# Kernel optimization log

Hardware: AMD Instinct MI355X
Metric: run time of the kernel (lower is better)

## Reference

```python
import jax, jax.numpy as jnp
import numpy as np

N_NODES = 50000
N_EDGES = 800000
IN_DIM = 128
HIDDEN_DIM = 128


def setup_inputs() -> dict:
    key = jax.random.key(0)
    k1, k2, k3, k4 = jax.random.split(key, 4)
    x = jax.random.normal(k1, (N_NODES, IN_DIM), dtype=jnp.float32)
    edge_index = jax.random.randint(k2, (2, N_EDGES), 0, N_NODES, dtype=jnp.int64)
    # Glorot-ish init for weights
    W1 = jax.random.normal(k3, (IN_DIM, HIDDEN_DIM), dtype=jnp.float32) / np.sqrt(IN_DIM)
    b1 = jnp.zeros((HIDDEN_DIM,), dtype=jnp.float32)
    W2 = jax.random.normal(k4, (HIDDEN_DIM, 2), dtype=jnp.float32) / np.sqrt(HIDDEN_DIM)
    b2 = jnp.zeros((2,), dtype=jnp.float32)
    return {"x": x, "edge_index": edge_index, "W1": W1, "b1": b1, "W2": W2, "b2": b2}


def _gcn_norm(edge_index, n_nodes):
    """Add self-loops and compute symmetric GCN normalization per edge."""
    loops = jnp.arange(n_nodes, dtype=edge_index.dtype)
    src = jnp.concatenate([edge_index[0], loops])  # [E + N]
    dst = jnp.concatenate([edge_index[1], loops])  # [E + N]
    ones = jnp.ones_like(dst, dtype=jnp.float32)
    deg = jax.ops.segment_sum(ones, dst, num_segments=n_nodes)  # [N]
    dinv = jnp.where(deg > 0, jax.lax.rsqrt(deg), 0.0)
    norm = dinv[src] * dinv[dst]  # [E + N]
    return src, dst, norm


def _gcn_conv(x, W, b, src, dst, norm, n_nodes):
    h = x @ W                                   # [N, out]
    msg = h[src] * norm[:, None]                # [E+N, out] gather + scale
    agg = jax.ops.segment_sum(msg, dst, num_segments=n_nodes)  # scatter-add
    return agg + b


def reference(x, edge_index, W1, b1, W2, b2):
    n = x.shape[0]
    src, dst, norm = _gcn_norm(edge_index, n)
    h = jax.nn.relu(_gcn_conv(x, W1, b1, src, dst, norm, n))
    out = _gcn_conv(h, W2, b2, src, dst, norm, n)
    return jax.nn.log_softmax(out, axis=1)
```

## Files before the change

kernel.cpp:

```cpp
#include <hip/hip_runtime.h>
#include <hip/hip_fp16.h>


#define DIM 128
#define SCAN_TILE 256

typedef _Float16 f16x8 __attribute__((ext_vector_type(8)));
typedef float f32x4 __attribute__((ext_vector_type(4)));

__device__ __forceinline__ int load_idx(const int* ei, long long pos, int is64) {
    if (is64) return (int)((const long long*)ei)[pos];
    return ei[pos];
}

__device__ __forceinline__ int detect_is64(const int* __restrict__ ei, int e) {
    __shared__ int sflag;
    int t = threadIdx.x;
    int hv = (t < 32 && (2 * t + 1) < 2 * e) ? ei[2 * t + 1] : 0;
    unsigned long long nz = __ballot(hv != 0);
    if (t == 0) sflag = (nz == 0ULL) ? 1 : 0;
    __syncthreads();
    return sflag;
}

__global__ void count_ticket_kernel(const int* __restrict__ ei, int* counts,
                                    int* __restrict__ s32, unsigned int* __restrict__ dt,
                                    int e) {
    int is64 = detect_is64(ei, e);
    int i = blockIdx.x * blockDim.x + threadIdx.x;
    if (i >= e) return;
    int s = load_idx(ei, i, is64);
    int d = load_idx(ei, (long long)e + i, is64);
    s32[i] = s;
    unsigned int tk = (unsigned int)atomicAdd(&counts[d], 1);
    dt[i] = (unsigned int)d | (tk << 17);
}

__global__ void fill_ticket_kernel(const int* __restrict__ s32, const unsigned int* __restrict__ dt,
                                   const int* __restrict__ row_ptr, int* __restrict__ col_idx,
                                   int e) {
    int i = blockIdx.x * blockDim.x + threadIdx.x;
    if (i >= e) return;
    unsigned int v = dt[i];
    int d = (int)(v & 0x1FFFFu);
    int tk = (int)(v >> 17);
    col_idx[row_ptr[d] + tk] = s32[i];
}

__global__ void count_kernel(const int* __restrict__ ei, int* counts, int e) {
    int is64 = detect_is64(ei, e);
    int i = blockIdx.x * blockDim.x + threadIdx.x;
    if (i >= e) return;
    int d = load_idx(ei, (long long)e + i, is64);
    atomicAdd(&counts[d], 1);
}

__global__ void fill_kernel(const int* __restrict__ ei, const int* __restrict__ row_ptr,
                            int* cursor, int* __restrict__ col_idx, int e) {
    int is64 = detect_is64(ei, e);
    int i = blockIdx.x * blockDim.x + threadIdx.x;
    if (i >= e) return;
    int s = load_idx(ei, i, is64);
    int d = load_idx(ei, (long long)e + i, is64);
    int pos = row_ptr[d] + atomicAdd(&cursor[d], 1);
    col_idx[pos] = s;
}

__global__ void scanA_kernel(const int* __restrict__ counts, int* __restrict__ tileSums, int n) {
    int t = threadIdx.x;
    int i = blockIdx.x * SCAN_TILE + t;
    int v = (i < n) ? counts[i] : 0;
    int lane = t & 63;
#pragma unroll
    for (int off = 32; off > 0; off >>= 1) v += __shfl_down(v, off);
    __shared__ int ws[4];
    if (lane == 0) ws[t >> 6] = v;
    __syncthreads();
    if (t == 0) tileSums[blockIdx.x] = ws[0] + ws[1] + ws[2] + ws[3];
}

#define TLP 136
__global__ void scanB_w1prep_kernel(int* tileSums, int ntiles,
                                    const float* __restrict__ W1, __half* __restrict__ W1T) {
    int t = threadIdx.x;
    int v = (t < ntiles) ? tileSums[t] : 0;
    int lane = t & 63, w = t >> 6;
    int x = v;
#pragma unroll
    for (int off = 1; off < 64; off <<= 1) {
        int y = __shfl_up(x, off);
        if (lane >= off) x += y;
    }
    __shared__ int ws[4];
    if (lane == 63) ws[w] = x;
    __syncthreads();
    int add = 0;
    for (int k = 0; k < w; ++k) add += ws[k];
    int incl = x + add;
    if (t < ntiles) tileSums[t] = incl - v;
    if (t == ntiles - 1) tileSums[ntiles] = incl;

    __shared__ __half tl[DIM * TLP];
    for (int i = 0; i < 64; ++i) {
        int f = t + i * 256;
        int k = f >> 7, c = f & 127;
        tl[c * TLP + k] = __float2half(W1[f]);
    }
    __syncthreads();
    for (int i = 0; i < 8; ++i) {
        int f = t + i * 256;
        int c = f >> 4, kc = f & 15;
        *(float4*)((char*)W1T + (size_t)f * 16) =
            *(float4*)((char*)tl + (size_t)c * (TLP * 2) + kc * 16);
    }
}

__global__ void scanC_kernel(const int* __restrict__ counts, const int* __restrict__ tileOff,
                             int* __restrict__ row_ptr, float* __restrict__ dinv, int n) {
    int t = threadIdx.x;
    int i = blockIdx.x * SCAN_TILE + t;
    int v = (i < n) ? counts[i] : 0;
    int lane = t & 63, w = t >> 6;
    int x = v;
#pragma unroll
    for (int off = 1; off < 64; off <<= 1) {
        int y = __shfl_up(x, off);
        if (lane >= off) x += y;
    }
    __shared__ int ws[4];
    if (lane == 63) ws[w] = x;
    __syncthreads();
    int add = tileOff[blockIdx.x];
    for (int k = 0; k < w; ++k) add += ws[k];
    if (i < n) {
        row_ptr[i] = add + x - v;
        dinv[i] = rsqrtf((float)(v + 1));
    }
    if (i == n - 1) row_ptr[n] = add + x;
}

#define GR 128
__global__ __launch_bounds__(256) void gemm1_kernel(
        const float* __restrict__ x, const __half* __restrict__ W1T,
        const float* __restrict__ dinv, __half* __restrict__ g1, int n) {
    __shared__ short xs[GR * DIM];
    __shared__ short wt[DIM * DIM];
    int t = threadIdx.x;
    int row0 = blockIdx.x * GR;

#pragma unroll
    for (int i = 0; i < 8; ++i) {
        int f = t + i * 256;
        int col = f >> 4, kc = f & 15;
        unsigned int byte = (unsigned)(col * 256 + kc * 16);
        byte ^= (unsigned)((col & 7) << 4);
        *(float4*)((char*)wt + byte) = *(const float4*)((const char*)W1T + (size_t)f * 16);
    }
#pragma unroll
    for (int i = 0; i < 16; ++i) {
        int f = t + i * 256;
        int r = f >> 5, c4 = f & 31;
        float4 v = make_float4(0.f, 0.f, 0.f, 0.f);
        if (row0 + r < n)
            v = *(const float4*)(x + (size_t)(row0 + r) * DIM + c4 * 4);
        __half2 p01 = __floats2half2_rn(v.x, v.y);
        __half2 p23 = __floats2half2_rn(v.z, v.w);
        float2 pk;
        ((__half2*)&pk)[0] = p01;
        ((__half2*)&pk)[1] = p23;
        unsigned int byte = (unsigned)(r * 256 + c4 * 8);
        byte ^= (unsigned)((r & 7) << 4);
        *(float2*)((char*)xs + byte) = pk;
    }
    __syncthreads();

    int w  = t >> 6;
    int l  = t & 63;
    int lr = l & 15;
    int lg = l >> 4;

    f32x4 acc[2][8];
#pragma unroll
    for (int m = 0; m < 2; ++m)
#pragma unroll
        for (int cf = 0; cf < 8; ++cf) acc[m][cf] = (f32x4){0.f, 0.f, 0.f, 0.f};

#pragma unroll
    for (int kt = 0; kt < 4; ++kt) {
        int kByte = kt * 64 + lg * 16;
        f16x8 a[2];
#pragma unroll
        for (int m = 0; m < 2; ++m) {
            int row = w * 32 + m * 16 + lr;
            unsigned int byte = (unsigned)(row * 256 + kByte);
            byte ^= (unsigned)((row & 7) << 4);
            a[m] = *(const f16x8*)((const char*)xs + byte);
        }
#pragma unroll
        for (int cf = 0; cf < 8; ++cf) {
            int col = cf * 16 + lr;
            unsigned int byte = (unsigned)(col * 256 + kByte);
            byte ^= (unsigned)((col & 7) << 4);
            f16x8 b = *(const f16x8*)((const char*)wt + byte);
            acc[0][cf] = __builtin_amdgcn_mfma_f32_16x16x32_f16(a[0], b, acc[0][cf], 0, 0, 0);
            acc[1][cf] = __builtin_amdgcn_mfma_f32_16x16x32_f16(a[1], b, acc[1][cf], 0, 0, 0);
        }
    }

    float dv[2][4];
#pragma unroll
    for (int m = 0; m < 2; ++m)
#pragma unroll
        for (int r4 = 0; r4 < 4; ++r4) {
            int row = row0 + w * 32 + m * 16 + lg * 4 + r4;
            dv[m][r4] = (row < n) ? dinv[row] : 0.f;
        }
#pragma unroll
    for (int m = 0; m < 2; ++m)
#pragma unroll
        for (int cf = 0; cf < 8; ++cf)
#pragma unroll
            for (int r4 = 0; r4 < 4; ++r4) {
                int row = row0 + w * 32 + m * 16 + lg * 4 + r4;
                if (row < n) {
                    int col = cf * 16 + lr;
                    g1[(size_t)row * DIM + col] = __float2half(acc[m][cf][r4] * dv[m][r4]);
                }
            }
}

__global__ void agg1_kernel(const __half* __restrict__ g1, const int* __restrict__ row_ptr,
                            const int* __restrict__ col_idx, const float* __restrict__ dinv,
                            const float* __restrict__ b1, const float* __restrict__ W2,
                            float* __restrict__ g2, int n) {
    int lane = threadIdx.x & 63;
    int wid  = threadIdx.x >> 6;
    int d = blockIdx.x * 4 + wid;
    if (d >= n) return;
    const __half2* base = (const __half2*)g1 + lane;
    float2 vf = __half22float2(base[d * 64]);
    float acc0 = vf.x, acc1 = vf.y;
    int beg = __builtin_amdgcn_readfirstlane(row_ptr[d]);
    int end = __builtin_amdgcn_readfirstlane(row_ptr[d + 1]);
    int j = beg;
    for (; j + 8 <= end; j += 8) {
        int s0 = col_idx[j + 0], s1 = col_idx[j + 1];
        int s2 = col_idx[j + 2], s3 = col_idx[j + 3];
        int s4 = col_idx[j + 4], s5 = col_idx[j + 5];
        int s6 = col_idx[j + 6], s7 = col_idx[j + 7];
        __half2 h0 = base[s0 * 64], h1 = base[s1 * 64];
        __half2 h2 = base[s2 * 64], h3 = base[s3 * 64];
        __half2 h4 = base[s4 * 64], h5 = base[s5 * 64];
        __half2 h6 = base[s6 * 64], h7 = base[s7 * 64];
        float2 u0 = __half22float2(h0), u1 = __half22float2(h1);
        float2 u2 = __half22float2(h2), u3 = __half22float2(h3);
        float2 u4 = __half22float2(h4), u5 = __half22float2(h5);
        float2 u6 = __half22float2(h6), u7 = __half22float2(h7);
        acc0 += ((u0.x + u1.x) + (u2.x + u3.x)) + ((u4.x + u5.x) + (u6.x + u7.x));
        acc1 += ((u0.y + u1.y) + (u2.y + u3.y)) + ((u4.y + u5.y) + (u6.y + u7.y));
    }
    for (; j < end; ++j) {
        float2 u = __half22float2(base[col_idx[j] * 64]);
        acc0 += u.x; acc1 += u.y;
    }
    float dv = dinv[d];
    int f0 = lane * 2, f1 = f0 + 1;
    float h0 = fmaxf(dv * acc0 + b1[f0], 0.f);
    float h1 = fmaxf(dv * acc1 + b1[f1], 0.f);
    float z0 = fmaf(h1, W2[f1 * 2 + 0], h0 * W2[f0 * 2 + 0]);
    float z1 = fmaf(h1, W2[f1 * 2 + 1], h0 * W2[f0 * 2 + 1]);
#pragma unroll
    for (int off = 32; off > 0; off >>= 1) {
        z0 += __shfl_down(z0, off);
        z1 += __shfl_down(z1, off);
    }
    if (lane == 0) {
        g2[d * 2 + 0] = dv * z0;
        g2[d * 2 + 1] = dv * z1;
    }
}

__global__ void agg2_kernel(const float* __restrict__ g2, const int* __restrict__ row_ptr,
                            const int* __restrict__ col_idx, const float* __restrict__ dinv,
                            const float* __restrict__ b2, float* __restrict__ out, int n) {
    int lane = threadIdx.x & 63;
    int wid  = threadIdx.x >> 6;
    int d = blockIdx.x * 4 + wid;
    if (d >= n) return;
    int beg = __builtin_amdgcn_readfirstlane(row_ptr[d]);
    int end = __builtin_amdgcn_readfirstlane(row_ptr[d + 1]);
    float a0 = 0.f, a1 = 0.f;
    const float2* g2v = (const float2*)g2;
    for (int j0 = beg; j0 < end; j0 += 64) {
        int j = j0 + lane;
        if (j < end) {
            float2 v = g2v[col_idx[j]];
            a0 += v.x; a1 += v.y;
        }
    }
#pragma unroll
    for (int off = 32; off > 0; off >>= 1) {
        a0 += __shfl_down(a0, off);
        a1 += __shfl_down(a1, off);
    }
    if (lane == 0) {
        float2 self = g2v[d];
        float dv = dinv[d];
        float z0 = dv * (a0 + self.x) + b2[0];
        float z1 = dv * (a1 + self.y) + b2[1];
        float m = fmaxf(z0, z1);
        float l = m + logf(expf(z0 - m) + expf(z1 - m));
        out[d * 2 + 0] = z0 - l;
        out[d * 2 + 1] = z1 - l;
    }
}

extern "C" void kernel_launch(void* const* d_in, const int* in_sizes, int n_in,
                              void* d_out, int out_size, void* d_ws, size_t ws_size,
                              hipStream_t stream) {
    const float* x  = (const float*)d_in[0];
    const int*   ei = (const int*)d_in[1];
    const float* W1 = (const float*)d_in[2];
    const float* b1 = (const float*)d_in[3];
    const float* W2 = (const float*)d_in[4];
    const float* b2 = (const float*)d_in[5];
    float* out = (float*)d_out;

    int n = in_sizes[0] / DIM;
    int e = in_sizes[1] / 2;
    int ntiles = (n + SCAN_TILE - 1) / SCAN_TILE;

    char* wsp = (char*)d_ws;
    size_t used = 0;
    auto alloc = [&](size_t bytes) {
        char* p = wsp + used;
        used += (bytes + 255) & ~(size_t)255;
        return p;
    };
    int*    counts   = (int*)alloc((size_t)n * 4);
    int*    cursor   = (int*)alloc((size_t)n * 4);
    int*    row_ptr  = (int*)alloc((size_t)(n + 1) * 4);
    int*    tileSums = (int*)alloc((size_t)(ntiles + 1) * 4);
    float*  dinv     = (float*)alloc((size_t)n * 4);
    int*    col_idx  = (int*)alloc((size_t)e * 4);
    __half* g1       = (__half*)alloc((size_t)n * DIM * 2);
    float*  g2       = (float*)alloc((size_t)n * 2 * 4);
    __half* W1T      = (__half*)alloc((size_t)DIM * DIM * 2);
    size_t zero_span = (size_t)((char*)row_ptr - (char*)counts);

    size_t per_e = ((size_t)e * 4 + 255) & ~(size_t)255;
    bool ticket_path = (used + 2 * per_e <= ws_size);
    int *s32 = nullptr; unsigned int* dt = nullptr;
    if (ticket_path) {
        s32 = (int*)alloc((size_t)e * 4);
        dt  = (unsigned int*)alloc((size_t)e * 4);
    }

    const int tb = 256;
    int eblk = (e + tb - 1) / tb;
    hipMemsetAsync(counts, 0, zero_span, stream);
    if (ticket_path)
        count_ticket_kernel<<<eblk, tb, 0, stream>>>(ei, counts, s32, dt, e);
    else
        count_kernel<<<eblk, tb, 0, stream>>>(ei, counts, e);
    scanA_kernel<<<ntiles, SCAN_TILE, 0, stream>>>(counts, tileSums, n);
    scanB_w1prep_kernel<<<1, 256, 0, stream>>>(tileSums, ntiles, W1, W1T);
    scanC_kernel<<<ntiles, SCAN_TILE, 0, stream>>>(counts, tileSums, row_ptr, dinv, n);
    if (ticket_path)
        fill_ticket_kernel<<<eblk, tb, 0, stream>>>(s32, dt, row_ptr, col_idx, e);
    else
        fill_kernel<<<eblk, tb, 0, stream>>>(ei, row_ptr, cursor, col_idx, e);
    gemm1_kernel<<<(n + GR - 1) / GR, 256, 0, stream>>>(x, W1T, dinv, g1, n);
    agg1_kernel<<<(n + 3) / 4, 256, 0, stream>>>(g1, row_ptr, col_idx, dinv, b1, W2, g2, n);
    agg2_kernel<<<(n + 3) / 4, 256, 0, stream>>>(g2, row_ptr, col_idx, dinv, b2, out, n);
}
```

Measured before the change: 129.2 us.

## Fuse CSR build into one cooperative kernel and narrow agg2 to 16 lanes

The memset, count, three-stage scan, W1 transpose and fill kernels are merged into a single cooperative kernel separated by grid.sync barriers. Each thread keeps its source, destination and ticket values in registers across the syncs, so the s32/dt scratch arrays and their global traffic go away. The W1 transpose is now split across four blocks. agg2 now gives each node 16 lanes instead of a full 64-lane wavefront, which suits the roughly 17 edges per node, and the gemm1 epilogue loads dinv per row inside the store loop. The cooperative launch needs every block resident at once, and each grid-wide barrier has its own cost.

New measurement: 487.7 us. +277.3%, slower.

```diff
diff --git a/kernel.cpp b/kernel.cpp
--- a/kernel.cpp
+++ b/kernel.cpp
@@ -1,142 +1,126 @@
 #include <hip/hip_runtime.h>
 #include <hip/hip_fp16.h>
+#include <hip/hip_cooperative_groups.h>
+
+namespace cg = cooperative_groups;
 
 
 #define DIM 128
-#define SCAN_TILE 256
+#define EPT 4
 
 typedef _Float16 f16x8 __attribute__((ext_vector_type(8)));
 typedef float f32x4 __attribute__((ext_vector_type(4)));
 
-__device__ __forceinline__ int load_idx(const int* ei, long long pos, int is64) {
-    if (is64) return (int)((const long long*)ei)[pos];
-    return ei[pos];
-}
-
-__device__ __forceinline__ int detect_is64(const int* __restrict__ ei, int e) {
+__global__ void __launch_bounds__(256) csr_coop_kernel(
+        const int* __restrict__ ei, const float* __restrict__ W1,
+        int* __restrict__ counts, int* __restrict__ tileSums,
+        int* __restrict__ row_ptr, float* __restrict__ dinv,
+        int* __restrict__ col_idx, __half* __restrict__ W1T,
+        int n, int e, int ntiles) {
+    cg::grid_group grid = cg::this_grid();
+    int t = threadIdx.x;
+    int tid = blockIdx.x * 256 + t;
+    int NT = gridDim.x * 256;
+
+    __shared__ __half wtile[32 * 136];
+    __shared__ int sred[4];
     __shared__ int sflag;
-    int t = threadIdx.x;
+
     int hv = (t < 32 && (2 * t + 1) < 2 * e) ? ei[2 * t + 1] : 0;
     unsigned long long nz = __ballot(hv != 0);
     if (t == 0) sflag = (nz == 0ULL) ? 1 : 0;
+
+    for (int i = tid; i < n; i += NT) counts[i] = 0;
     __syncthreads();
-    return sflag;
-}
-
-__global__ void count_ticket_kernel(const int* __restrict__ ei, int* counts,
-                                    int* __restrict__ s32, unsigned int* __restrict__ dt,
-                                    int e) {
-    int is64 = detect_is64(ei, e);
-    int i = blockIdx.x * blockDim.x + threadIdx.x;
-    if (i >= e) return;
-    int s = load_idx(ei, i, is64);
-    int d = load_idx(ei, (long long)e + i, is64);
-    s32[i] = s;
-    unsigned int tk = (unsigned int)atomicAdd(&counts[d], 1);
-    dt[i] = (unsigned int)d | (tk << 17);
-}
-
-__global__ void fill_ticket_kernel(const int* __restrict__ s32, const unsigned int* __restrict__ dt,
-                                   const int* __restrict__ row_ptr, int* __restrict__ col_idx,
-                                   int e) {
-    int i = blockIdx.x * blockDim.x + threadIdx.x;
-    if (i >= e) return;
-    unsigned int v = dt[i];
-    int d = (int)(v & 0x1FFFFu);
-    int tk = (int)(v >> 17);
-    col_idx[row_ptr[d] + tk] = s32[i];
-}
-
-__global__ void count_kernel(const int* __restrict__ ei, int* counts, int e) {
-    int is64 = detect_is64(ei, e);
-    int i = blockIdx.x * blockDim.x + threadIdx.x;
-    if (i >= e) return;
-    int d = load_idx(ei, (long long)e + i, is64);
-    atomicAdd(&counts[d], 1);
-}
-
-__global__ void fill_kernel(const int* __restrict__ ei, const int* __restrict__ row_ptr,
-                            int* cursor, int* __restrict__ col_idx, int e) {
-    int is64 = detect_is64(ei, e);
-    int i = blockIdx.x * blockDim.x + threadIdx.x;
-    if (i >= e) return;
-    int s = load_idx(ei, i, is64);
-    int d = load_idx(ei, (long long)e + i, is64);
-    int pos = row_ptr[d] + atomicAdd(&cursor[d], 1);
-    col_idx[pos] = s;
-}
-
-__global__ void scanA_kernel(const int* __restrict__ counts, int* __restrict__ tileSums, int n) {
-    int t = threadIdx.x;
-    int i = blockIdx.x * SCAN_TILE + t;
-    int v = (i < n) ? counts[i] : 0;
-    int lane = t & 63;
-#pragma unroll
-    for (int off = 32; off > 0; off >>= 1) v += __shfl_down(v, off);
-    __shared__ int ws[4];
-    if (lane == 0) ws[t >> 6] = v;
-    __syncthreads();
-    if (t == 0) tileSums[blockIdx.x] = ws[0] + ws[1] + ws[2] + ws[3];
-}
-
-#define TLP 136
-__global__ void scanB_w1prep_kernel(int* tileSums, int ntiles,
-                                    const float* __restrict__ W1, __half* __restrict__ W1T) {
-    int t = threadIdx.x;
-    int v = (t < ntiles) ? tileSums[t] : 0;
-    int lane = t & 63, w = t >> 6;
-    int x = v;
-#pragma unroll
-    for (int off = 1; off < 64; off <<= 1) {
-        int y = __shfl_up(x, off);
-        if (lane >= off) x += y;
-    }
-    __shared__ int ws[4];
-    if (lane == 63) ws[w] = x;
-    __syncthreads();
-    int add = 0;
-    for (int k = 0; k < w; ++k) add += ws[k];
-    int incl = x + add;
-    if (t < ntiles) tileSums[t] = incl - v;
-    if (t == ntiles - 1) tileSums[ntiles] = incl;
-
-    __shared__ __half tl[DIM * TLP];
-    for (int i = 0; i < 64; ++i) {
-        int f = t + i * 256;
-        int k = f >> 7, c = f & 127;
-        tl[c * TLP + k] = __float2half(W1[f]);
-    }
-    __syncthreads();
-    for (int i = 0; i < 8; ++i) {
-        int f = t + i * 256;
-        int c = f >> 4, kc = f & 15;
-        *(float4*)((char*)W1T + (size_t)f * 16) =
-            *(float4*)((char*)tl + (size_t)c * (TLP * 2) + kc * 16);
-    }
-}
-
-__global__ void scanC_kernel(const int* __restrict__ counts, const int* __restrict__ tileOff,
-                             int* __restrict__ row_ptr, float* __restrict__ dinv, int n) {
-    int t = threadIdx.x;
-    int i = blockIdx.x * SCAN_TILE + t;
-    int v = (i < n) ? counts[i] : 0;
-    int lane = t & 63, w = t >> 6;
-    int x = v;
-#pragma unroll
-    for (int off = 1; off < 64; off <<= 1) {
-        int y = __shfl_up(x, off);
-        if (lane >= off) x += y;
-    }
-    __shared__ int ws[4];
-    if (lane == 63) ws[w] = x;
-    __syncthreads();
-    int add = tileOff[blockIdx.x];
-    for (int k = 0; k < w; ++k) add += ws[k];
-    if (i < n) {
-        row_ptr[i] = add + x - v;
-        dinv[i] = rsqrtf((float)(v + 1));
-    }
-    if (i == n - 1) row_ptr[n] = add + x;
+    int is64 = sflag;
+    grid.sync();
+
+    int se[EPT], de[EPT], tk[EPT];
+    long long base = (long long)tid * EPT;
+#pragma unroll
+    for (int k = 0; k < EPT; ++k) {
+        long long idx = base + k;
+        if (idx < e) {
+            se[k] = is64 ? (int)((const long long*)ei)[idx] : ei[idx];
+            de[k] = is64 ? (int)((const long long*)ei)[e + idx] : ei[e + idx];
+            tk[k] = atomicAdd(&counts[de[k]], 1);
+        }
+    }
+    grid.sync();
+
+    if (blockIdx.x < ntiles) {
+        int i = blockIdx.x * 256 + t;
+        int v = (i < n) ? counts[i] : 0;
+        int lane = t & 63;
+#pragma unroll
+        for (int off = 32; off > 0; off >>= 1) v += __shfl_down(v, off);
+        if (lane == 0) sred[t >> 6] = v;
+        __syncthreads();
+        if (t == 0) tileSums[blockIdx.x] = sred[0] + sred[1] + sred[2] + sred[3];
+    }
+    grid.sync();
+
+    if (blockIdx.x == 0) {
+        int v = (t < ntiles) ? tileSums[t] : 0;
+        int lane = t & 63, w = t >> 6;
+        int x = v;
+#pragma unroll
+        for (int off = 1; off < 64; off <<= 1) {
+            int y = __shfl_up(x, off);
+            if (lane >= off) x += y;
+        }
+        if (lane == 63) sred[w] = x;
+        __syncthreads();
+        int add = 0;
+        for (int k = 0; k < w; ++k) add += sred[k];
+        int incl = x + add;
+        if (t < ntiles) tileSums[t] = incl - v;
+        if (t == ntiles - 1) tileSums[ntiles] = incl;
+    } else if (blockIdx.x <= 4) {
+        int c0 = (blockIdx.x - 1) * 32;
+        for (int it = 0; it < 16; ++it) {
+            int k = it * 8 + (t >> 5);
+            int c = t & 31;
+            wtile[c * 136 + k] = __float2half(W1[(size_t)k * DIM + c0 + c]);
+        }
+        __syncthreads();
+#pragma unroll
+        for (int it = 0; it < 2; ++it) {
+            int c = t >> 3;
+            int kc = (t & 7) + it * 8;
+            *(float4*)((char*)(W1T + (size_t)(c0 + c) * DIM) + kc * 16) =
+                *(float4*)((char*)(wtile + c * 136) + kc * 16);
+        }
+    }
+    grid.sync();
+
+    if (blockIdx.x < ntiles) {
+        int i = blockIdx.x * 256 + t;
+        int v = (i < n) ? counts[i] : 0;
+        int lane = t & 63, w = t >> 6;
+        int x = v;
+#pragma unroll
+        for (int off = 1; off < 64; off <<= 1) {
+            int y = __shfl_up(x, off);
+            if (lane >= off) x += y;
+        }
+        if (lane == 63) sred[w] = x;
+        __syncthreads();
+        int add = tileSums[blockIdx.x];
+        for (int k = 0; k < w; ++k) add += sred[k];
+        if (i < n) {
+            row_ptr[i] = add + x - v;
+            dinv[i] = rsqrtf((float)(v + 1));
+        }
+        if (i == n - 1) row_ptr[n] = add + x;
+    }
+    grid.sync();
+
+#pragma unroll
+    for (int k = 0; k < EPT; ++k) {
+        long long idx = base + k;
+        if (idx < e) col_idx[row_ptr[de[k]] + tk[k]] = se[k];
+    }
 }
 
 #define GR 128
@@ -207,26 +191,20 @@
         }
     }
 
-    float dv[2][4];
 #pragma unroll
     for (int m = 0; m < 2; ++m)
 #pragma unroll
         for (int r4 = 0; r4 < 4; ++r4) {
             int row = row0 + w * 32 + m * 16 + lg * 4 + r4;
-            dv[m][r4] = (row < n) ? dinv[row] : 0.f;
-        }
-#pragma unroll
-    for (int m = 0; m < 2; ++m)
-#pragma unroll
-        for (int cf = 0; cf < 8; ++cf)
-#pragma unroll
-            for (int r4 = 0; r4 < 4; ++r4) {
-                int row = row0 + w * 32 + m * 16 + lg * 4 + r4;
-                if (row < n) {
+            if (row < n) {
+                float dv = dinv[row];
+#pragma unroll
+                for (int cf = 0; cf < 8; ++cf) {
                     int col = cf * 16 + lr;
-                    g1[(size_t)row * DIM + col] = __float2half(acc[m][cf][r4] * dv[m][r4]);
+                    g1[(size_t)row * DIM + col] = __float2half(acc[m][cf][r4] * dv);
                 }
             }
+        }
 }
 
 __global__ void agg1_kernel(const __half* __restrict__ g1, const int* __restrict__ row_ptr,
@@ -283,27 +261,23 @@
 __global__ void agg2_kernel(const float* __restrict__ g2, const int* __restrict__ row_ptr,
                             const int* __restrict__ col_idx, const float* __restrict__ dinv,
                             const float* __restrict__ b2, float* __restrict__ out, int n) {
-    int lane = threadIdx.x & 63;
-    int wid  = threadIdx.x >> 6;
-    int d = blockIdx.x * 4 + wid;
+    int t = threadIdx.x;
+    int sub = t & 15;
+    int d = blockIdx.x * 16 + (t >> 4);
     if (d >= n) return;
-    int beg = __builtin_amdgcn_readfirstlane(row_ptr[d]);
-    int end = __builtin_amdgcn_readfirstlane(row_ptr[d + 1]);
+    int beg = row_ptr[d], end = row_ptr[d + 1];
     float a0 = 0.f, a1 = 0.f;
     const float2* g2v = (const float2*)g2;
-    for (int j0 = beg; j0 < end; j0 += 64) {
-        int j = j0 + lane;
-        if (j < end) {
-            float2 v = g2v[col_idx[j]];
-            a0 += v.x; a1 += v.y;
-        }
-    }
-#pragma unroll
-    for (int off = 32; off > 0; off >>= 1) {
-        a0 += __shfl_down(a0, off);
-        a1 += __shfl_down(a1, off);
-    }
-    if (lane == 0) {
+    for (int j = beg + sub; j < end; j += 16) {
+        float2 v = g2v[col_idx[j]];
+        a0 += v.x; a1 += v.y;
+    }
+#pragma unroll
+    for (int off = 8; off > 0; off >>= 1) {
+        a0 += __shfl_down(a0, off, 16);
+        a1 += __shfl_down(a1, off, 16);
+    }
+    if (sub == 0) {
         float2 self = g2v[d];
         float dv = dinv[d];
         float z0 = dv * (a0 + self.x) + b2[0];
@@ -328,7 +302,7 @@
 
     int n = in_sizes[0] / DIM;
     int e = in_sizes[1] / 2;
-    int ntiles = (n + SCAN_TILE - 1) / SCAN_TILE;
+    int ntiles = (n + 255) / 256;
 
     char* wsp = (char*)d_ws;
     size_t used = 0;
@@ -338,7 +312,6 @@
         return p;
     };
     int*    counts   = (int*)alloc((size_t)n * 4);
-    int*    cursor   = (int*)alloc((size_t)n * 4);
     int*    row_ptr  = (int*)alloc((size_t)(n + 1) * 4);
     int*    tileSums = (int*)alloc((size_t)(ntiles + 1) * 4);
     float*  dinv     = (float*)alloc((size_t)n * 4);
@@ -346,31 +319,18 @@
     __half* g1       = (__half*)alloc((size_t)n * DIM * 2);
     float*  g2       = (float*)alloc((size_t)n * 2 * 4);
     __half* W1T      = (__half*)alloc((size_t)DIM * DIM * 2);
-    size_t zero_span = (size_t)((char*)row_ptr - (char*)counts);
-
-    size_t per_e = ((size_t)e * 4 + 255) & ~(size_t)255;
-    bool ticket_path = (used + 2 * per_e <= ws_size);
-    int *s32 = nullptr; unsigned int* dt = nullptr;
-    if (ticket_path) {
-        s32 = (int*)alloc((size_t)e * 4);
-        dt  = (unsigned int*)alloc((size_t)e * 4);
-    }
-
-    const int tb = 256;
-    int eblk = (e + tb - 1) / tb;
-    hipMemsetAsync(counts, 0, zero_span, stream);
-    if (ticket_path)
-        count_ticket_kernel<<<eblk, tb, 0, stream>>>(ei, counts, s32, dt, e);
-    else
-        count_kernel<<<eblk, tb, 0, stream>>>(ei, counts, e);
-    scanA_kernel<<<ntiles, SCAN_TILE, 0, stream>>>(counts, tileSums, n);
-    scanB_w1prep_kernel<<<1, 256, 0, stream>>>(tileSums, ntiles, W1, W1T);
-    scanC_kernel<<<ntiles, SCAN_TILE, 0, stream>>>(counts, tileSums, row_ptr, dinv, n);
-    if (ticket_path)
-        fill_ticket_kernel<<<eblk, tb, 0, stream>>>(s32, dt, row_ptr, col_idx, e);
-    else
-        fill_kernel<<<eblk, tb, 0, stream>>>(ei, row_ptr, cursor, col_idx, e);
+
+    int nblk = (e + 256 * EPT - 1) / (256 * EPT);
+    if (nblk < ntiles) nblk = ntiles;
+    if (nblk < 5) nblk = 5;
+
+    void* args[] = {(void*)&ei, (void*)&W1, (void*)&counts, (void*)&tileSums,
+                    (void*)&row_ptr, (void*)&dinv, (void*)&col_idx, (void*)&W1T,
+                    (void*)&n, (void*)&e, (void*)&ntiles};
+    hipLaunchCooperativeKernel((const void*)csr_coop_kernel, dim3(nblk), dim3(256),
+                               args, 0, stream);
+
     gemm1_kernel<<<(n + GR - 1) / GR, 256, 0, stream>>>(x, W1T, dinv, g1, n);
     agg1_kernel<<<(n + 3) / 4, 256, 0, stream>>>(g1, row_ptr, col_idx, dinv, b1, W2, g2, n);
-    agg2_kernel<<<(n + 3) / 4, 256, 0, stream>>>(g2, row_ptr, col_idx, dinv, b2, out, n);
-}
+    agg2_kernel<<<(n + 15) / 16, 256, 0, stream>>>(g2, row_ptr, col_idx, dinv, b2, out, n);
+}
```
